# Performance work log

Hardware: AMD Instinct MI355X
Metric: run time of the kernel (lower is better)

The kernel has to match this reference:

```python
import jax, jax.numpy as jnp
import numpy as np

N = 512     # nodes
E = 16384   # edges (N * avg_degree 32, unique pairs)
F = 64      # nedgeinput
FO = 64     # nedgeoutput


def setup_inputs() -> dict:
    key = jax.random.key(0)
    ks = jax.random.split(key, 7)
    # unique edge pairs so scatter-assign is well-defined
    perm = jax.random.permutation(ks[0], N * N)[:E]
    edge_index = jnp.stack([perm // N, perm % N]).astype(jnp.int32)  # [2, E]
    C = jax.random.normal(ks[1], (E, F), dtype=jnp.float32)
    batch_node = jax.random.normal(ks[2], (N,), dtype=jnp.float32)
    s = 1.0 / np.sqrt(F)
    W_L1 = jax.random.normal(ks[3], (F, F), dtype=jnp.float32) * s          # Linear(F, F), weight [out,in]
    W_L2 = jax.random.normal(ks[4], (F, F), dtype=jnp.float32) * s
    W_mlp1 = jax.random.normal(ks[5], (8 * F, 2 * F), dtype=jnp.float32) * (1.0 / np.sqrt(2 * F))
    W_mlp2 = jax.random.normal(ks[6], (FO, 8 * F), dtype=jnp.float32) * (1.0 / np.sqrt(8 * F))
    return {"edge_index": edge_index, "C": C, "batch_node": batch_node,
            "W_L1": W_L1, "W_L2": W_L2, "W_mlp1": W_mlp1, "W_mlp2": W_mlp2}


def reference(edge_index, C, batch_node, W_L1, W_L2, W_mlp1, W_mlp2):
    n = batch_node.shape[0]
    f = C.shape[1]
    ei0, ei1 = edge_index[0], edge_index[1]
    X = C @ W_L1.T  # [E, F]  (L1(C))
    Y = C @ W_L2.T  # [E, F]  (L2(C))
    # scatter edges into dense [F, N, N] adjacency-like tensors
    resx = jnp.zeros((f, n, n), dtype=C.dtype).at[:, ei0, ei1].set(X.T)
    resy = jnp.zeros((f, n, n), dtype=C.dtype).at[:, ei0, ei1].set(Y.T)
    # batched dense matmul per feature channel, then gather back at edges
    res = jnp.einsum('fij,fjk->fik', resx, resy)  # [F, N, N]
    tmp_matmul = res[:, ei0, ei1].T  # [E, F]
    tmp = jnp.concatenate([C, tmp_matmul], axis=1)  # [E, 2F]
    return jax.nn.relu(tmp @ W_mlp1.T) @ W_mlp2.T  # [E, FO]
```

## Files before the change

### kernel.cpp

```cpp
#include <hip/hip_runtime.h>

#define NN 512
#define NE 16384
#define NF 64

typedef __attribute__((ext_vector_type(8))) short short8_t;
typedef __attribute__((ext_vector_type(4))) float float4_t;

__device__ inline unsigned short f2bf(float f) {
  unsigned u = __builtin_bit_cast(unsigned, f);
  u += 0x7fff + ((u >> 16) & 1);
  return (unsigned short)(u >> 16);
}
__device__ inline float bf2f(unsigned short u) {
  unsigned v = ((unsigned)u) << 16;
  return __builtin_bit_cast(float, v);
}

__global__ __launch_bounds__(256) void k_xy_mfma(const float* __restrict__ C,
                                                 const float* __restrict__ W1,
                                                 const float* __restrict__ W2,
                                                 const int* __restrict__ ei,
                                                 int* __restrict__ eid,
                                                 unsigned* __restrict__ maskO,
                                                 unsigned* __restrict__ maskI,
                                                 unsigned short* __restrict__ Xb,
                                                 unsigned short* __restrict__ Yb) {
  __shared__ __attribute__((aligned(16))) short W1s[64 * 72];
  __shared__ __attribute__((aligned(16))) short W2s[64 * 72];
  int t = threadIdx.x;
  int w = t >> 6;
  int lane = t & 63;
  int col = lane & 15;
  int q = lane >> 4;
  int base_e = blockIdx.x * 64 + w * 16;

  if (t < 64) {
    int e = blockIdx.x * 64 + t;
    int i = ei[e];
    int k = ei[NE + e];
    eid[i * NN + k] = e;
    atomicOr(&maskO[i * 16 + (k >> 5)], 1u << (k & 31));
    atomicOr(&maskI[k * 16 + (i >> 5)], 1u << (i & 31));
  }

#pragma unroll
  for (int z = 0; z < 4; z++) {
    int gi = z * 256 + t;
    int r = gi >> 4, c = gi & 15;
    float4 v1 = ((const float4*)W1)[r * 16 + c];
    float4 v2 = ((const float4*)W2)[r * 16 + c];
    short4 s1, s2;
    s1.x = f2bf(v1.x); s1.y = f2bf(v1.y); s1.z = f2bf(v1.z); s1.w = f2bf(v1.w);
    s2.x = f2bf(v2.x); s2.y = f2bf(v2.y); s2.z = f2bf(v2.z); s2.w = f2bf(v2.w);
    *(short4*)(W1s + r * 72 + c * 4) = s1;
    *(short4*)(W2s + r * 72 + c * 4) = s2;
  }
  __syncthreads();

  short8_t bfrag[2];
#pragma unroll
  for (int ks = 0; ks < 2; ks++) {
    float4 c0 = ((const float4*)C)[(size_t)(base_e + col) * 16 + ks * 8 + q * 2];
    float4 c1 = ((const float4*)C)[(size_t)(base_e + col) * 16 + ks * 8 + q * 2 + 1];
    short8_t s;
    s[0] = (short)f2bf(c0.x); s[1] = (short)f2bf(c0.y);
    s[2] = (short)f2bf(c0.z); s[3] = (short)f2bf(c0.w);
    s[4] = (short)f2bf(c1.x); s[5] = (short)f2bf(c1.y);
    s[6] = (short)f2bf(c1.z); s[7] = (short)f2bf(c1.w);
    bfrag[ks] = s;
  }

  float4_t xa[4], ya[4];
#pragma unroll
  for (int ft = 0; ft < 4; ft++) {
    xa[ft] = (float4_t){0.f, 0.f, 0.f, 0.f};
    ya[ft] = (float4_t){0.f, 0.f, 0.f, 0.f};
  }
#pragma unroll
  for (int ks = 0; ks < 2; ks++) {
#pragma unroll
    for (int ft = 0; ft < 4; ft++) {
      short8_t a1 = *(const short8_t*)(W1s + (ft * 16 + col) * 72 + ks * 32 + q * 8);
      short8_t a2 = *(const short8_t*)(W2s + (ft * 16 + col) * 72 + ks * 32 + q * 8);
      xa[ft] = __builtin_amdgcn_mfma_f32_16x16x32_bf16(a1, bfrag[ks], xa[ft], 0, 0, 0);
      ya[ft] = __builtin_amdgcn_mfma_f32_16x16x32_bf16(a2, bfrag[ks], ya[ft], 0, 0, 0);
    }
  }
#pragma unroll
  for (int ft = 0; ft < 4; ft++) {
    short4 sx, sy;
    sx.x = (short)f2bf(xa[ft][0]); sx.y = (short)f2bf(xa[ft][1]);
    sx.z = (short)f2bf(xa[ft][2]); sx.w = (short)f2bf(xa[ft][3]);
    sy.x = (short)f2bf(ya[ft][0]); sy.y = (short)f2bf(ya[ft][1]);
    sy.z = (short)f2bf(ya[ft][2]); sy.w = (short)f2bf(ya[ft][3]);
    *(short4*)(Xb + (size_t)(base_e + col) * 64 + ft * 16 + q * 4) = sx;
    *(short4*)(Yb + (size_t)(base_e + col) * 64 + ft * 16 + q * 4) = sy;
  }
}

__global__ __launch_bounds__(256) void k_spmm(const int* __restrict__ ei,
                                              const int* __restrict__ eid,
                                              const unsigned* __restrict__ maskO,
                                              const unsigned* __restrict__ maskI,
                                              const unsigned short* __restrict__ Xb,
                                              const unsigned short* __restrict__ Yb,
                                              const float* __restrict__ Wm1,
                                              const float* __restrict__ Wm2,
                                              unsigned short* __restrict__ W1B,
                                              unsigned short* __restrict__ W2B,
                                              unsigned short* __restrict__ tmpB) {
  __shared__ int jl[4][512];
  int lane = threadIdx.x & 63;
  int w = threadIdx.x >> 6;
  int e = (blockIdx.x * 256 + threadIdx.x) >> 6;
  int i = ei[e];
  int k = ei[NE + e];

  if (blockIdx.x < 96) {
    int t4 = blockIdx.x * 256 + threadIdx.x;
    if (t4 < 16384) {
      float4 v = ((const float4*)Wm1)[t4];
      short4 s;
      s.x = f2bf(v.x); s.y = f2bf(v.y); s.z = f2bf(v.z); s.w = f2bf(v.w);
      ((short4*)W1B)[t4] = s;
    } else {
      int i2 = t4 - 16384;
      float4 v = ((const float4*)Wm2)[i2];
      short4 s;
      s.x = f2bf(v.x); s.y = f2bf(v.y); s.z = f2bf(v.z); s.w = f2bf(v.w);
      ((short4*)W2B)[i2] = s;
    }
  }

  unsigned mm = 0;
  if (lane < 16) mm = maskO[i * 16 + lane] & maskI[k * 16 + lane];

  int mcnt = __popc(mm);
  int incl = mcnt;
#pragma unroll
  for (int d = 1; d < 16; d <<= 1) {
    int y = __shfl_up(incl, d);
    if (lane >= d) incl += y;
  }
  int off = incl - mcnt;
  int cnt = __shfl(incl, 15);
  unsigned bits = mm;
  while (bits) {
    int b = __builtin_ctz(bits);
    bits &= bits - 1;
    jl[w][off++] = lane * 32 + b;
  }
  __syncthreads();

  float acc = 0.f;
  for (int base = 0; base < cnt; base += 8) {
    int idx[8], s1[8], s2[8];
#pragma unroll
    for (int b = 0; b < 8; b++) {
      int t = base + b;
      idx[b] = jl[w][t < cnt ? t : base];
    }
#pragma unroll
    for (int b = 0; b < 8; b++) {
      s1[b] = eid[i * NN + idx[b]];
      s2[b] = eid[idx[b] * NN + k];
    }
    float xv[8], yv[8];
#pragma unroll
    for (int b = 0; b < 8; b++) {
      xv[b] = bf2f(Xb[(size_t)s1[b] * 64 + lane]);
      yv[b] = bf2f(Yb[(size_t)s2[b] * 64 + lane]);
    }
#pragma unroll
    for (int b = 0; b < 8; b++) {
      if (base + b < cnt) acc = fmaf(xv[b], yv[b], acc);
    }
  }
  tmpB[(size_t)e * 128 + 64 + lane] = f2bf(acc);
}

__global__ __launch_bounds__(256) void k_mlp2(
    const float* __restrict__ C,
    const unsigned short* __restrict__ tmpB,
    const unsigned short* __restrict__ W1B,
    const unsigned short* __restrict__ W2B,
    float* __restrict__ out) {
  __shared__ __attribute__((aligned(16))) short W1s[128 * 136];
  __shared__ __attribute__((aligned(16))) short W2s[64 * 136];
  __shared__ __attribute__((aligned(16))) short hS[4][16 * 72];

  int t = threadIdx.x;
  int w = t >> 6;
  int lane = t & 63;
  int col = lane & 15;
  int q = lane >> 4;
  int g = w & 1;
  int h = w >> 1;
  int base_e = blockIdx.x * 32 + g * 16;

  short8_t btmp[4];
#pragma unroll
  for (int ks = 0; ks < 2; ks++) {
    float4 c0 = ((const float4*)C)[(size_t)(base_e + col) * 16 + ks * 8 + q * 2];
    float4 c1 = ((const float4*)C)[(size_t)(base_e + col) * 16 + ks * 8 + q * 2 + 1];
    short8_t s;
    s[0] = (short)f2bf(c0.x); s[1] = (short)f2bf(c0.y);
    s[2] = (short)f2bf(c0.z); s[3] = (short)f2bf(c0.w);
    s[4] = (short)f2bf(c1.x); s[5] = (short)f2bf(c1.y);
    s[6] = (short)f2bf(c1.z); s[7] = (short)f2bf(c1.w);
    btmp[ks] = s;
  }
#pragma unroll
  for (int ks = 2; ks < 4; ks++)
    btmp[ks] = *(const short8_t*)(tmpB + (size_t)(base_e + col) * 128 + ks * 32 + q * 8);

  float4_t oacc[4];
#pragma unroll
  for (int ft = 0; ft < 4; ft++) oacc[ft] = (float4_t){0.f, 0.f, 0.f, 0.f};

  for (int it = 0; it < 4; it++) {
    __syncthreads();
    {
      uint4* d1 = (uint4*)W1s;
      const uint4* s1 = (const uint4*)W1B;
#pragma unroll
      for (int z = 0; z < 8; z++) {
        int gi = z * 256 + t;
        int r = gi >> 4, c = gi & 15;
        int grow = ((r >> 6) * 4 + it) * 64 + (r & 63);
        d1[r * 17 + c] = s1[(size_t)grow * 16 + c];
      }
      uint4* d2 = (uint4*)W2s;
      const uint4* s2 = (const uint4*)W2B;
#pragma unroll
      for (int z = 0; z < 4; z++) {
        int gi = z * 256 + t;
        int r = gi >> 4, c = gi & 15;
        int gc = ((c >> 3) * 4 + it) * 8 + (c & 7);
        d2[r * 17 + c] = s2[(size_t)r * 64 + gc];
      }
    }
    __syncthreads();

#pragma unroll
    for (int ht = 0; ht < 4; ht++) {
      float4_t hacc = (float4_t){0.f, 0.f, 0.f, 0.f};
#pragma unroll
      for (int ks = 0; ks < 4; ks++) {
        short8_t af = *(const short8_t*)(W1s + (h * 64 + ht * 16 + col) * 136 + ks * 32 + q * 8);
        hacc = __builtin_amdgcn_mfma_f32_16x16x32_bf16(af, btmp[ks], hacc, 0, 0, 0);
      }
      short4 hp;
      hp.x = (short)f2bf(fmaxf(hacc[0], 0.f));
      hp.y = (short)f2bf(fmaxf(hacc[1], 0.f));
      hp.z = (short)f2bf(fmaxf(hacc[2], 0.f));
      hp.w = (short)f2bf(fmaxf(hacc[3], 0.f));
      *(short4*)(&hS[w][col * 72 + ht * 16 + q * 4]) = hp;
    }

#pragma unroll
    for (int ks2 = 0; ks2 < 2; ks2++) {
      short8_t a2 = *(const short8_t*)(&hS[w][col * 72 + ks2 * 32 + q * 8]);
#pragma unroll
      for (int ft = 0; ft < 4; ft++) {
        short8_t b2 = *(const short8_t*)(W2s + (ft * 16 + col) * 136 + h * 64 + ks2 * 32 + q * 8);
        oacc[ft] = __builtin_amdgcn_mfma_f32_16x16x32_bf16(a2, b2, oacc[ft], 0, 0, 0);
      }
    }
  }

  __syncthreads();
  float* red = (float*)W1s;
  if (h == 1) {
#pragma unroll
    for (int ft = 0; ft < 4; ft++)
#pragma unroll
      for (int r = 0; r < 4; r++)
        red[(g * 16 + q * 4 + r) * 66 + ft * 16 + col] = oacc[ft][r];
  }
  __syncthreads();
  if (h == 0) {
#pragma unroll
    for (int ft = 0; ft < 4; ft++)
#pragma unroll
      for (int r = 0; r < 4; r++) {
        float v = oacc[ft][r] + red[(g * 16 + q * 4 + r) * 66 + ft * 16 + col];
        out[(size_t)(base_e + q * 4 + r) * 64 + ft * 16 + col] = v;
      }
  }
}

extern "C" void kernel_launch(void* const* d_in, const int* in_sizes, int n_in,
                              void* d_out, int out_size, void* d_ws, size_t ws_size,
                              hipStream_t stream) {
  const int* ei = (const int*)d_in[0];
  const float* C = (const float*)d_in[1];
  const float* W1 = (const float*)d_in[3];
  const float* W2 = (const float*)d_in[4];
  const float* Wm1 = (const float*)d_in[5];
  const float* Wm2 = (const float*)d_in[6];
  float* out = (float*)d_out;

  char* p = (char*)d_ws;
  int* eid = (int*)p;                 p += (size_t)NN * NN * 4;
  unsigned* masks = (unsigned*)p;     p += (size_t)16384 * 4;
  unsigned short* Xb = (unsigned short*)p;    p += (size_t)NE * NF * 2;
  unsigned short* Yb = (unsigned short*)p;    p += (size_t)NE * NF * 2;
  unsigned short* tmpB = (unsigned short*)p;  p += (size_t)NE * 128 * 2;
  unsigned short* W1B = (unsigned short*)p;   p += (size_t)512 * 128 * 2;
  unsigned short* W2B = (unsigned short*)p;   p += (size_t)64 * 512 * 2;
  unsigned* maskO = masks;
  unsigned* maskI = masks + 8192;

  hipMemsetAsync(masks, 0, 16384 * sizeof(unsigned), stream);
  k_xy_mfma<<<NE / 64, 256, 0, stream>>>(C, W1, W2, ei, eid, maskO, maskI, Xb, Yb);
  k_spmm<<<(NE * 64) / 256, 256, 0, stream>>>(ei, eid, maskO, maskI, Xb, Yb,
                                              Wm1, Wm2, W1B, W2B, tmpB);
  k_mlp2<<<NE / 32, 256, 0, stream>>>(C, tmpB, W1B, W2B, out);
}
```

Measured before the change: 96.46 us.

## Fuse sparse triangle product into MLP kernel and move weight conversion earlier

Merges the sparse common-neighbour product into the MLP kernel, which now uses 512-thread blocks of 64 edges. The per-edge result stays in shared memory instead of going through a global tmpB buffer. The bf16 conversion of the MLP weights moves into the first kernel, and the sparse loop now gives each edge 16 lanes that fetch short4 slices, with neighbour ids gathered through shuffles. This removes one launch and a global write/read round trip. In exchange it uses much more LDS per block, which lowers occupancy, and it caps the common-neighbour list at 128 entries.

```diff
diff --git a/kernel.cpp b/kernel.cpp
--- a/kernel.cpp
+++ b/kernel.cpp
@@ -21,11 +21,15 @@
                                                  const float* __restrict__ W1,
                                                  const float* __restrict__ W2,
                                                  const int* __restrict__ ei,
+                                                 const float* __restrict__ Wm1,
+                                                 const float* __restrict__ Wm2,
                                                  int* __restrict__ eid,
                                                  unsigned* __restrict__ maskO,
                                                  unsigned* __restrict__ maskI,
                                                  unsigned short* __restrict__ Xb,
-                                                 unsigned short* __restrict__ Yb) {
+                                                 unsigned short* __restrict__ Yb,
+                                                 unsigned short* __restrict__ W1B,
+                                                 unsigned short* __restrict__ W2B) {
   __shared__ __attribute__((aligned(16))) short W1s[64 * 72];
   __shared__ __attribute__((aligned(16))) short W2s[64 * 72];
   int t = threadIdx.x;
@@ -44,81 +48,8 @@
     atomicOr(&maskI[k * 16 + (i >> 5)], 1u << (i & 31));
   }
 
-#pragma unroll
-  for (int z = 0; z < 4; z++) {
-    int gi = z * 256 + t;
-    int r = gi >> 4, c = gi & 15;
-    float4 v1 = ((const float4*)W1)[r * 16 + c];
-    float4 v2 = ((const float4*)W2)[r * 16 + c];
-    short4 s1, s2;
-    s1.x = f2bf(v1.x); s1.y = f2bf(v1.y); s1.z = f2bf(v1.z); s1.w = f2bf(v1.w);
-    s2.x = f2bf(v2.x); s2.y = f2bf(v2.y); s2.z = f2bf(v2.z); s2.w = f2bf(v2.w);
-    *(short4*)(W1s + r * 72 + c * 4) = s1;
-    *(short4*)(W2s + r * 72 + c * 4) = s2;
-  }
-  __syncthreads();
-
-  short8_t bfrag[2];
-#pragma unroll
-  for (int ks = 0; ks < 2; ks++) {
-    float4 c0 = ((const float4*)C)[(size_t)(base_e + col) * 16 + ks * 8 + q * 2];
-    float4 c1 = ((const float4*)C)[(size_t)(base_e + col) * 16 + ks * 8 + q * 2 + 1];
-    short8_t s;
-    s[0] = (short)f2bf(c0.x); s[1] = (short)f2bf(c0.y);
-    s[2] = (short)f2bf(c0.z); s[3] = (short)f2bf(c0.w);
-    s[4] = (short)f2bf(c1.x); s[5] = (short)f2bf(c1.y);
-    s[6] = (short)f2bf(c1.z); s[7] = (short)f2bf(c1.w);
-    bfrag[ks] = s;
-  }
-
-  float4_t xa[4], ya[4];
-#pragma unroll
-  for (int ft = 0; ft < 4; ft++) {
-    xa[ft] = (float4_t){0.f, 0.f, 0.f, 0.f};
-    ya[ft] = (float4_t){0.f, 0.f, 0.f, 0.f};
-  }
-#pragma unroll
-  for (int ks = 0; ks < 2; ks++) {
-#pragma unroll
-    for (int ft = 0; ft < 4; ft++) {
-      short8_t a1 = *(const short8_t*)(W1s + (ft * 16 + col) * 72 + ks * 32 + q * 8);
-      short8_t a2 = *(const short8_t*)(W2s + (ft * 16 + col) * 72 + ks * 32 + q * 8);
-      xa[ft] = __builtin_amdgcn_mfma_f32_16x16x32_bf16(a1, bfrag[ks], xa[ft], 0, 0, 0);
-      ya[ft] = __builtin_amdgcn_mfma_f32_16x16x32_bf16(a2, bfrag[ks], ya[ft], 0, 0, 0);
-    }
-  }
-#pragma unroll
-  for (int ft = 0; ft < 4; ft++) {
-    short4 sx, sy;
-    sx.x = (short)f2bf(xa[ft][0]); sx.y = (short)f2bf(xa[ft][1]);
-    sx.z = (short)f2bf(xa[ft][2]); sx.w = (short)f2bf(xa[ft][3]);
-    sy.x = (short)f2bf(ya[ft][0]); sy.y = (short)f2bf(ya[ft][1]);
-    sy.z = (short)f2bf(ya[ft][2]); sy.w = (short)f2bf(ya[ft][3]);
-    *(short4*)(Xb + (size_t)(base_e + col) * 64 + ft * 16 + q * 4) = sx;
-    *(short4*)(Yb + (size_t)(base_e + col) * 64 + ft * 16 + q * 4) = sy;
-  }
-}
-
-__global__ __launch_bounds__(256) void k_spmm(const int* __restrict__ ei,
-                                              const int* __restrict__ eid,
-                                              const unsigned* __restrict__ maskO,
-                                              const unsigned* __restrict__ maskI,
-                                              const unsigned short* __restrict__ Xb,
-                                              const unsigned short* __restrict__ Yb,
-                                              const float* __restrict__ Wm1,
-                                              const float* __restrict__ Wm2,
-                                              unsigned short* __restrict__ W1B,
-                                              unsigned short* __restrict__ W2B,
-                                              unsigned short* __restrict__ tmpB) {
-  __shared__ int jl[4][512];
-  int lane = threadIdx.x & 63;
-  int w = threadIdx.x >> 6;
-  int e = (blockIdx.x * 256 + threadIdx.x) >> 6;
-  int i = ei[e];
-  int k = ei[NE + e];
-
-  if (blockIdx.x < 96) {
-    int t4 = blockIdx.x * 256 + threadIdx.x;
+  if (t >= 64 && t < 160) {
+    int t4 = blockIdx.x * 96 + (t - 64);
     if (t4 < 16384) {
       float4 v = ((const float4*)Wm1)[t4];
       short4 s;
@@ -133,71 +64,153 @@
     }
   }
 
-  unsigned mm = 0;
-  if (lane < 16) mm = maskO[i * 16 + lane] & maskI[k * 16 + lane];
-
-  int mcnt = __popc(mm);
-  int incl = mcnt;
-#pragma unroll
-  for (int d = 1; d < 16; d <<= 1) {
-    int y = __shfl_up(incl, d);
-    if (lane >= d) incl += y;
-  }
-  int off = incl - mcnt;
-  int cnt = __shfl(incl, 15);
-  unsigned bits = mm;
-  while (bits) {
-    int b = __builtin_ctz(bits);
-    bits &= bits - 1;
-    jl[w][off++] = lane * 32 + b;
+#pragma unroll
+  for (int z = 0; z < 4; z++) {
+    int gi = z * 256 + t;
+    int r = gi >> 4, c = gi & 15;
+    float4 v1 = ((const float4*)W1)[r * 16 + c];
+    float4 v2 = ((const float4*)W2)[r * 16 + c];
+    short4 s1, s2;
+    s1.x = f2bf(v1.x); s1.y = f2bf(v1.y); s1.z = f2bf(v1.z); s1.w = f2bf(v1.w);
+    s2.x = f2bf(v2.x); s2.y = f2bf(v2.y); s2.z = f2bf(v2.z); s2.w = f2bf(v2.w);
+    *(short4*)(W1s + r * 72 + c * 4) = s1;
+    *(short4*)(W2s + r * 72 + c * 4) = s2;
   }
   __syncthreads();
 
-  float acc = 0.f;
-  for (int base = 0; base < cnt; base += 8) {
-    int idx[8], s1[8], s2[8];
-#pragma unroll
-    for (int b = 0; b < 8; b++) {
-      int t = base + b;
-      idx[b] = jl[w][t < cnt ? t : base];
-    }
-#pragma unroll
-    for (int b = 0; b < 8; b++) {
-      s1[b] = eid[i * NN + idx[b]];
-      s2[b] = eid[idx[b] * NN + k];
-    }
-    float xv[8], yv[8];
-#pragma unroll
-    for (int b = 0; b < 8; b++) {
-      xv[b] = bf2f(Xb[(size_t)s1[b] * 64 + lane]);
-      yv[b] = bf2f(Yb[(size_t)s2[b] * 64 + lane]);
-    }
-#pragma unroll
-    for (int b = 0; b < 8; b++) {
-      if (base + b < cnt) acc = fmaf(xv[b], yv[b], acc);
-    }
-  }
-  tmpB[(size_t)e * 128 + 64 + lane] = f2bf(acc);
-}
-
-__global__ __launch_bounds__(256) void k_mlp2(
+  short8_t bfrag[2];
+#pragma unroll
+  for (int ks = 0; ks < 2; ks++) {
+    float4 c0 = ((const float4*)C)[(size_t)(base_e + col) * 16 + ks * 8 + q * 2];
+    float4 c1 = ((const float4*)C)[(size_t)(base_e + col) * 16 + ks * 8 + q * 2 + 1];
+    short8_t s;
+    s[0] = (short)f2bf(c0.x); s[1] = (short)f2bf(c0.y);
+    s[2] = (short)f2bf(c0.z); s[3] = (short)f2bf(c0.w);
+    s[4] = (short)f2bf(c1.x); s[5] = (short)f2bf(c1.y);
+    s[6] = (short)f2bf(c1.z); s[7] = (short)f2bf(c1.w);
+    bfrag[ks] = s;
+  }
+
+  float4_t xa[4], ya[4];
+#pragma unroll
+  for (int ft = 0; ft < 4; ft++) {
+    xa[ft] = (float4_t){0.f, 0.f, 0.f, 0.f};
+    ya[ft] = (float4_t){0.f, 0.f, 0.f, 0.f};
+  }
+#pragma unroll
+  for (int ks = 0; ks < 2; ks++) {
+#pragma unroll
+    for (int ft = 0; ft < 4; ft++) {
+      short8_t a1 = *(const short8_t*)(W1s + (ft * 16 + col) * 72 + ks * 32 + q * 8);
+      short8_t a2 = *(const short8_t*)(W2s + (ft * 16 + col) * 72 + ks * 32 + q * 8);
+      xa[ft] = __builtin_amdgcn_mfma_f32_16x16x32_bf16(a1, bfrag[ks], xa[ft], 0, 0, 0);
+      ya[ft] = __builtin_amdgcn_mfma_f32_16x16x32_bf16(a2, bfrag[ks], ya[ft], 0, 0, 0);
+    }
+  }
+#pragma unroll
+  for (int ft = 0; ft < 4; ft++) {
+    short4 sx, sy;
+    sx.x = (short)f2bf(xa[ft][0]); sx.y = (short)f2bf(xa[ft][1]);
+    sx.z = (short)f2bf(xa[ft][2]); sx.w = (short)f2bf(xa[ft][3]);
+    sy.x = (short)f2bf(ya[ft][0]); sy.y = (short)f2bf(ya[ft][1]);
+    sy.z = (short)f2bf(ya[ft][2]); sy.w = (short)f2bf(ya[ft][3]);
+    *(short4*)(Xb + (size_t)(base_e + col) * 64 + ft * 16 + q * 4) = sx;
+    *(short4*)(Yb + (size_t)(base_e + col) * 64 + ft * 16 + q * 4) = sy;
+  }
+}
+
+__global__ __launch_bounds__(512) void k_spmlp(
+    const int* __restrict__ ei,
+    const int* __restrict__ eid,
+    const unsigned* __restrict__ maskO,
+    const unsigned* __restrict__ maskI,
+    const unsigned short* __restrict__ Xb,
+    const unsigned short* __restrict__ Yb,
     const float* __restrict__ C,
-    const unsigned short* __restrict__ tmpB,
     const unsigned short* __restrict__ W1B,
     const unsigned short* __restrict__ W2B,
     float* __restrict__ out) {
   __shared__ __attribute__((aligned(16))) short W1s[128 * 136];
   __shared__ __attribute__((aligned(16))) short W2s[64 * 136];
-  __shared__ __attribute__((aligned(16))) short hS[4][16 * 72];
+  __shared__ __attribute__((aligned(16))) short hS[8][16 * 72];
+  __shared__ __attribute__((aligned(16))) short tm[64 * 72];
+  __shared__ unsigned short jl16[64][128];
 
   int t = threadIdx.x;
   int w = t >> 6;
   int lane = t & 63;
+  int gl = lane & 15;
+  int grp = lane >> 4;
+
+#pragma unroll
+  for (int round = 0; round < 2; round++) {
+    int le = round * 32 + w * 4 + grp;
+    int e = blockIdx.x * 64 + le;
+    int i = ei[e];
+    int k = ei[NE + e];
+    unsigned mm = maskO[i * 16 + gl] & maskI[k * 16 + gl];
+
+    int mcnt = __popc(mm);
+    int incl = mcnt;
+#pragma unroll
+    for (int d = 1; d < 16; d <<= 1) {
+      int y = __shfl(incl, (lane & 48) | ((gl - d) & 15));
+      if (gl >= d) incl += y;
+    }
+    int off = incl - mcnt;
+    int cnt = __shfl(incl, (lane & 48) | 15);
+
+    unsigned bits = mm;
+    while (bits) {
+      int b = __builtin_ctz(bits);
+      bits &= bits - 1;
+      if (off < 128) jl16[le][off] = (unsigned short)(gl * 32 + b);
+      off++;
+    }
+    if (cnt > 128) cnt = 128;
+
+    float acc0 = 0.f, acc1 = 0.f, acc2 = 0.f, acc3 = 0.f;
+    for (int base = 0; base < cnt; base += 8) {
+      int b = gl & 7;
+      int t2 = base + b;
+      int jj = jl16[le][t2 < cnt ? t2 : base];
+      int addr = (gl < 8) ? (i * NN + jj) : (jj * NN + k);
+      int sv = eid[addr];
+      short4 xs[8], ys[8];
+#pragma unroll
+      for (int b2 = 0; b2 < 8; b2++) {
+        int s1 = __shfl(sv, (lane & 48) | b2);
+        int s2 = __shfl(sv, (lane & 48) | (8 + b2));
+        xs[b2] = *(const short4*)(Xb + (size_t)s1 * 64 + gl * 4);
+        ys[b2] = *(const short4*)(Yb + (size_t)s2 * 64 + gl * 4);
+      }
+#pragma unroll
+      for (int b2 = 0; b2 < 8; b2++) {
+        if (base + b2 < cnt) {
+          acc0 = fmaf(bf2f((unsigned short)xs[b2].x), bf2f((unsigned short)ys[b2].x), acc0);
+          acc1 = fmaf(bf2f((unsigned short)xs[b2].y), bf2f((unsigned short)ys[b2].y), acc1);
+          acc2 = fmaf(bf2f((unsigned short)xs[b2].z), bf2f((unsigned short)ys[b2].z), acc2);
+          acc3 = fmaf(bf2f((unsigned short)xs[b2].w), bf2f((unsigned short)ys[b2].w), acc3);
+        }
+      }
+    }
+    short4 o4;
+    o4.x = (short)f2bf(acc0);
+    o4.y = (short)f2bf(acc1);
+    o4.z = (short)f2bf(acc2);
+    o4.w = (short)f2bf(acc3);
+    *(short4*)(tm + le * 72 + gl * 4) = o4;
+  }
+  __syncthreads();
+
+  int u = w >> 2;
+  int wl = w & 3;
+  int g = wl & 1;
+  int h = wl >> 1;
   int col = lane & 15;
   int q = lane >> 4;
-  int g = w & 1;
-  int h = w >> 1;
-  int base_e = blockIdx.x * 32 + g * 16;
+  int base_e = blockIdx.x * 64 + u * 32 + g * 16;
+  int le0 = u * 32 + g * 16 + col;
 
   short8_t btmp[4];
 #pragma unroll
@@ -213,7 +226,7 @@
   }
 #pragma unroll
   for (int ks = 2; ks < 4; ks++)
-    btmp[ks] = *(const short8_t*)(tmpB + (size_t)(base_e + col) * 128 + ks * 32 + q * 8);
+    btmp[ks] = *(const short8_t*)(tm + le0 * 72 + (ks - 2) * 32 + q * 8);
 
   float4_t oacc[4];
 #pragma unroll
@@ -225,8 +238,8 @@
       uint4* d1 = (uint4*)W1s;
       const uint4* s1 = (const uint4*)W1B;
 #pragma unroll
-      for (int z = 0; z < 8; z++) {
-        int gi = z * 256 + t;
+      for (int z = 0; z < 4; z++) {
+        int gi = z * 512 + t;
         int r = gi >> 4, c = gi & 15;
         int grow = ((r >> 6) * 4 + it) * 64 + (r & 63);
         d1[r * 17 + c] = s1[(size_t)grow * 16 + c];
@@ -234,8 +247,8 @@
       uint4* d2 = (uint4*)W2s;
       const uint4* s2 = (const uint4*)W2B;
 #pragma unroll
-      for (int z = 0; z < 4; z++) {
-        int gi = z * 256 + t;
+      for (int z = 0; z < 2; z++) {
+        int gi = z * 512 + t;
         int r = gi >> 4, c = gi & 15;
         int gc = ((c >> 3) * 4 + it) * 8 + (c & 7);
         d2[r * 17 + c] = s2[(size_t)r * 64 + gc];
@@ -277,7 +290,7 @@
     for (int ft = 0; ft < 4; ft++)
 #pragma unroll
       for (int r = 0; r < 4; r++)
-        red[(g * 16 + q * 4 + r) * 66 + ft * 16 + col] = oacc[ft][r];
+        red[(u * 32 + g * 16 + q * 4 + r) * 66 + ft * 16 + col] = oacc[ft][r];
   }
   __syncthreads();
   if (h == 0) {
@@ -285,7 +298,7 @@
     for (int ft = 0; ft < 4; ft++)
 #pragma unroll
       for (int r = 0; r < 4; r++) {
-        float v = oacc[ft][r] + red[(g * 16 + q * 4 + r) * 66 + ft * 16 + col];
+        float v = oacc[ft][r] + red[(u * 32 + g * 16 + q * 4 + r) * 66 + ft * 16 + col];
         out[(size_t)(base_e + q * 4 + r) * 64 + ft * 16 + col] = v;
       }
   }
@@ -307,15 +320,14 @@
   unsigned* masks = (unsigned*)p;     p += (size_t)16384 * 4;
   unsigned short* Xb = (unsigned short*)p;    p += (size_t)NE * NF * 2;
   unsigned short* Yb = (unsigned short*)p;    p += (size_t)NE * NF * 2;
-  unsigned short* tmpB = (unsigned short*)p;  p += (size_t)NE * 128 * 2;
   unsigned short* W1B = (unsigned short*)p;   p += (size_t)512 * 128 * 2;
   unsigned short* W2B = (unsigned short*)p;   p += (size_t)64 * 512 * 2;
   unsigned* maskO = masks;
   unsigned* maskI = masks + 8192;
 
   hipMemsetAsync(masks, 0, 16384 * sizeof(unsigned), stream);
-  k_xy_mfma<<<NE / 64, 256, 0, stream>>>(C, W1, W2, ei, eid, maskO, maskI, Xb, Yb);
-  k_spmm<<<(NE * 64) / 256, 256, 0, stream>>>(ei, eid, maskO, maskI, Xb, Yb,
-                                              Wm1, Wm2, W1B, W2B, tmpB);
-  k_mlp2<<<NE / 32, 256, 0, stream>>>(C, tmpB, W1B, W2B, out);
-}
+  k_xy_mfma<<<NE / 64, 256, 0, stream>>>(C, W1, W2, ei, Wm1, Wm2, eid,
+                                         maskO, maskI, Xb, Yb, W1B, W2B);
+  k_spmlp<<<NE / 64, 512, 0, stream>>>(ei, eid, maskO, maskI, Xb, Yb,
+                                       C, W1B, W2B, out);
+}
```

Measured after the change: 91.07 us. -5.6%, faster.
